# Performance work log

Hardware: AMD Instinct MI355X
Metric: run time of the kernel (lower is better)

Reference implementation:

```python
import jax, jax.numpy as jnp
import numpy as np
from jax import lax

K = 3
K2 = 9
PAD = 1
GN_GROUPS = 32
GN_EPS = 1e-5
COS_EPS = 1e-8


def conv2d(x, w):
    # 3x3, stride 1, pad 1, NCHW/OIHW
    return lax.conv_general_dilated(x, w, (1, 1), ((PAD, PAD), (PAD, PAD)),
                                    dimension_numbers=('NCHW', 'OIHW', 'NCHW'))


def group_norm(x, gamma, beta):
    N, C, H, W = x.shape
    xg = x.reshape(N, GN_GROUPS, C // GN_GROUPS, H, W)
    m = xg.mean(axis=(2, 3, 4), keepdims=True)
    v = xg.var(axis=(2, 3, 4), keepdims=True)
    xn = ((xg - m) * lax.rsqrt(v + GN_EPS)).reshape(N, C, H, W)
    return xn * gamma[None, :, None, None] + beta[None, :, None, None]


def deform_conv(x, offset, weight):
    # mmcv DeformConv, deformable_groups=1: offset [N, 2*K2, H, W] as (dy,dx) per kernel tap.
    N, C, H, W = x.shape
    off = offset.reshape(N, K2, 2, H, W)
    dy, dx = off[:, :, 0], off[:, :, 1]              # [N,K2,H,W]
    ky, kx = jnp.meshgrid(jnp.arange(K), jnp.arange(K), indexing='ij')
    ky = ky.reshape(K2).astype(x.dtype)
    kx = kx.reshape(K2).astype(x.dtype)
    hh = jnp.arange(H, dtype=x.dtype)
    ww = jnp.arange(W, dtype=x.dtype)
    # absolute (fractional) sample positions per output pixel and kernel tap
    py = hh[None, None, :, None] - PAD + ky[None, :, None, None] + dy   # [N,K2,H,W]
    px = ww[None, None, None, :] - PAD + kx[None, :, None, None] + dx
    y0 = jnp.floor(py)
    x0 = jnp.floor(px)
    ay = py - y0
    ax = px - x0
    xf = x.reshape(N, C, H * W)
    sampled = jnp.zeros((N, C, K2, H, W), x.dtype)
    for oy, wy in ((y0, 1.0 - ay), (y0 + 1.0, ay)):
        for ox, wx in ((x0, 1.0 - ax), (x0 + 1.0, ax)):
            valid = (oy >= 0) & (oy <= H - 1) & (ox >= 0) & (ox <= W - 1)
            yi = jnp.clip(oy, 0, H - 1).astype(jnp.int32)
            xi = jnp.clip(ox, 0, W - 1).astype(jnp.int32)
            idx = (yi * W + xi).reshape(N, 1, K2 * H * W)
            v = jnp.take_along_axis(xf, idx, axis=2).reshape(N, C, K2, H, W)
            w = jnp.where(valid, wy * wx, 0.0)[:, None]   # zero padding outside
            sampled = sampled + v * w
    O = weight.shape[0]
    return jnp.einsum('nckhw,ock->nohw', sampled, weight.reshape(O, C, K2))


def cos_sim(a, b):
    num = jnp.sum(a * b, axis=1)
    na = jnp.sqrt(jnp.sum(a * a, axis=1))
    nb = jnp.sqrt(jnp.sum(b * b, axis=1))
    return num / jnp.maximum(na * nb, COS_EPS)   # [N,H,W]


def agg(support, reference, layers):
    f = jnp.concatenate([support, reference], axis=1)
    for ow, ob, dw, gg, gb in layers[:3]:
        off = conv2d(f, ow) + ob[None, :, None, None]
        f = jax.nn.relu(group_norm(deform_conv(f, off, dw), gg, gb))
    ow, ob, dw, gg, gb = layers[3]
    off = conv2d(f, ow) + ob[None, :, None, None]
    return jax.nn.relu(group_norm(deform_conv(support, off, dw), gg, gb))


def setup_inputs() -> dict:
    key = jax.random.key(0)
    ks = jax.random.split(key, 16)
    C_in, C_out, H, W = 512, 256, 96, 96
    rn = lambda k, shape, s: jax.random.normal(k, shape, jnp.float32) * s
    inp = {'datas': jax.random.normal(ks[0], (2, C_out, H, W), jnp.float32)}
    i = 1
    for n in (1, 2, 3):
        inp[f'off{n}_w'] = rn(ks[i], (18, C_in, 3, 3), 0.01); i += 1
        inp[f'off{n}_b'] = jnp.zeros((18,), jnp.float32)
        inp[f'dcn{n}_w'] = rn(ks[i], (C_in, C_in, 3, 3), 0.02); i += 1
        inp[f'gn{n}_g'] = jnp.ones((C_in,), jnp.float32)
        inp[f'gn{n}_b'] = jnp.zeros((C_in,), jnp.float32)
    inp['off4_w'] = rn(ks[i], (18, C_in, 3, 3), 0.01); i += 1
    inp['off4_b'] = jnp.zeros((18,), jnp.float32)
    inp['dcn4_w'] = rn(ks[i], (C_out, C_out, 3, 3), 0.02); i += 1
    inp['gn4_g'] = jnp.ones((C_out,), jnp.float32)
    inp['gn4_b'] = jnp.zeros((C_out,), jnp.float32)
    return inp


def reference(datas, off1_w, off1_b, dcn1_w, gn1_g, gn1_b,
              off2_w, off2_b, dcn2_w, gn2_g, gn2_b,
              off3_w, off3_b, dcn3_w, gn3_g, gn3_b,
              off4_w, off4_b, dcn4_w, gn4_g, gn4_b):
    layers = [(off1_w, off1_b, dcn1_w, gn1_g, gn1_b),
              (off2_w, off2_b, dcn2_w, gn2_g, gn2_b),
              (off3_w, off3_b, dcn3_w, gn3_g, gn3_b),
              (off4_w, off4_b, dcn4_w, gn4_g, gn4_b)]
    support = datas[:1]
    reference_f = datas[1:]
    tt = agg(reference_f, reference_f, layers)   # [1,C_out,H,W]
    ttw = cos_sim(tt, tt)[:, None]               # [1,1,H,W]
    tk = agg(support, reference_f, layers)
    tkw = cos_sim(tt, tk)[:, None]
    w = jax.nn.softmax(jnp.stack([ttw, tkw], axis=0), axis=0)  # [2,1,1,H,W]
    f = jnp.stack([tt, tk], axis=0)                            # [2,1,C,H,W]
    return jnp.sum(w * f, axis=0)
```

## Files before the change

### kernel.cpp

```cpp
#include <hip/hip_runtime.h>
#include <math.h>

#define HW 9216
#define WIDTH 96
#define FSTRIDE (512*HW)
#define RSTRIDE (256*HW)
#define TABSTRIDE (9*HW)
#define PXP 12544
#define FTPROWS 12800

typedef __attribute__((ext_vector_type(8))) short bf16x8;
typedef __attribute__((ext_vector_type(4))) float f32x4;
typedef __attribute__((ext_vector_type(8))) unsigned short u16x8;

__device__ __forceinline__ unsigned short f2bf(float f) {
  unsigned int u = __float_as_uint(f);
  u += 0x7FFFu + ((u >> 16) & 1u);
  return (unsigned short)(u >> 16);
}
__device__ __forceinline__ float bf2f(unsigned short s) {
  return __uint_as_float(((unsigned int)s) << 16);
}

#define GLDS(g, l) __builtin_amdgcn_global_load_lds( \
    (const __attribute__((address_space(1))) unsigned int*)(g), \
    (__attribute__((address_space(3))) unsigned int*)(l), 16, 0, 0)

__global__ void k_zero(unsigned short* p, unsigned int n8) {
  unsigned int i = blockIdx.x * 256 + threadIdx.x;
  if (i < n8) ((u16x8*)p)[i] = (u16x8){0, 0, 0, 0, 0, 0, 0, 0};
}

__global__ void __launch_bounds__(256) k_mkftp_cat(
    const float* __restrict__ lo0, const float* __restrict__ lo1,
    const float* __restrict__ hi, unsigned short* __restrict__ dst,
    int C, int CB) {
  const int b = blockIdx.z;
  const float* lo = b ? lo1 : lo0;
  unsigned short* d = dst + (size_t)b * FTPROWS * C + 128 * C;
  const int px0 = blockIdx.x * 64, c0 = blockIdx.y * 64;
  __shared__ float tile[64][65];
  const int t = threadIdx.x;
#pragma unroll
  for (int rep = 0; rep < 16; ++rep) {
    int idx = rep * 256 + t;
    int cl = idx >> 6, pl = idx & 63;
    int cg = c0 + cl;
    const float* s = (cg < CB) ? (lo + (size_t)cg * HW) : (hi + (size_t)(cg - CB) * HW);
    tile[cl][pl] = s[px0 + pl];
  }
  __syncthreads();
  const int pl = t >> 2, cu = (t & 3) * 16;
  const int px = px0 + pl;
  const int h = px / WIDTH, w = px - h * WIDTH;
  const size_t pxp = (size_t)(h + 1) * 128 + (w + 1);
  u16x8 o0, o1;
#pragma unroll
  for (int j = 0; j < 8; ++j) o0[j] = f2bf(tile[cu + j][pl]);
#pragma unroll
  for (int j = 0; j < 8; ++j) o1[j] = f2bf(tile[cu + 8 + j][pl]);
  unsigned short* p = d + pxp * C + c0 + cu;
  *(u16x8*)p = o0;
  *(u16x8*)(p + 8) = o1;
}

__global__ void __launch_bounds__(256) k_mkftp_gn(
    const unsigned short* __restrict__ yh, const float2* __restrict__ stat,
    const float* __restrict__ gamma, const float* __restrict__ beta,
    unsigned short* __restrict__ dst) {
  const int C = 512;
  const int b = blockIdx.z;
  unsigned short* d = dst + (size_t)b * FTPROWS * C + 128 * C;
  const int px0 = blockIdx.x * 64, c0 = blockIdx.y * 64;
  __shared__ float tile[64][65];
  const int t = threadIdx.x;
#pragma unroll
  for (int rep = 0; rep < 16; ++rep) {
    int idx = rep * 256 + t;
    int cl = idx >> 6, pl = idx & 63;
    int cg = c0 + cl;
    float2 st = stat[b * 32 + (cg >> 4)];
    float v = bf2f(yh[(size_t)b * FSTRIDE + (size_t)cg * HW + px0 + pl]);
    v = (v - st.x) * st.y * gamma[cg] + beta[cg];
    tile[cl][pl] = fmaxf(v, 0.f);
  }
  __syncthreads();
  const int pl = t >> 2, cu = (t & 3) * 16;
  const int px = px0 + pl;
  const int h = px / WIDTH, w = px - h * WIDTH;
  const size_t pxp = (size_t)(h + 1) * 128 + (w + 1);
  u16x8 o0, o1;
#pragma unroll
  for (int j = 0; j < 8; ++j) o0[j] = f2bf(tile[cu + j][pl]);
#pragma unroll
  for (int j = 0; j < 8; ++j) o1[j] = f2bf(tile[cu + 8 + j][pl]);
  unsigned short* p = d + pxp * C + c0 + cu;
  *(u16x8*)p = o0;
  *(u16x8*)(p + 8) = o1;
}

__global__ void k_prepW(const float* __restrict__ ow, unsigned short* __restrict__ Wt) {
  int i = blockIdx.x * 256 + threadIdx.x;
  int k = i / (32 * 512), r = i - k * 32 * 512;
  int oc = r / 512, c = r - oc * 512;
  Wt[i] = (oc < 18) ? f2bf(ow[((size_t)oc * 512 + c) * 9 + k]) : (unsigned short)0;
}

__global__ void __launch_bounds__(256) k_offmm(const unsigned short* __restrict__ ftp,
                                               const unsigned short* __restrict__ Wt,
                                               float* __restrict__ part) {
  const int C = 512;
  __shared__ unsigned short As[2][128 * 64];
  __shared__ unsigned short Bs[2][32 * 64];
  const int tid = threadIdx.x;
  const int lane = tid & 63, wv = tid >> 6;
  const int b = blockIdx.z, ks = blockIdx.y;
  const int pxp0 = 128 + blockIdx.x * 128;
  const unsigned short* fb = ftp + (size_t)b * FTPROWS * C + 128 * C;

  const int lr = lane >> 3;
  const int lu = lane & 7;
  const int fr = lane & 15, hi = lane >> 4;

  f32x4 acc[2][2];
#pragma unroll
  for (int i = 0; i < 2; ++i)
#pragma unroll
    for (int j = 0; j < 2; ++j) acc[i][j] = (f32x4){0.f, 0.f, 0.f, 0.f};

#define OFFMM_STAGE(S, BUF)                                                   \
  {                                                                           \
    const int k_ = ks * 3 + ((S) >> 3);                                       \
    const int dlt_ = (k_ / 3 - 1) * 128 + (k_ % 3 - 1);                       \
    const int c0_ = ((S) & 7) * 64;                                           \
    _Pragma("unroll")                                                         \
    for (int q = 0; q < 4; ++q) {                                             \
      int row = wv * 32 + q * 8 + lr;                                         \
      int su = lu ^ (row & 7);                                                \
      GLDS(fb + (size_t)(pxp0 + dlt_ + row) * C + c0_ + su * 8,               \
           (char*)&As[BUF][0] + (wv * 32 + q * 8) * 128);                     \
    }                                                                         \
    {                                                                         \
      int row = wv * 8 + lr;                                                  \
      int su = lu ^ (row & 7);                                                \
      GLDS(Wt + ((size_t)k_ * 32 + row) * C + c0_ + su * 8,                   \
           (char*)&Bs[BUF][0] + wv * 8 * 128);                                \
    }                                                                         \
  }

  OFFMM_STAGE(0, 0);
  for (int s = 0; s < 24; ++s) {
    const int cur = s & 1;
    if (s + 1 < 24) {
      OFFMM_STAGE(s + 1, cur ^ 1);
      asm volatile("s_waitcnt vmcnt(5)" ::: "memory");
    } else {
      asm volatile("s_waitcnt vmcnt(0)" ::: "memory");
    }
    __builtin_amdgcn_s_barrier();
#pragma unroll
    for (int kk = 0; kk < 2; ++kk) {
      bf16x8 a[2], bb[2];
#pragma unroll
      for (int i = 0; i < 2; ++i) {
        int row = wv * 32 + i * 16 + fr;
        a[i] = *(const bf16x8*)&As[cur][row * 64 + (((kk * 4 + hi) ^ (row & 7)) * 8)];
      }
#pragma unroll
      for (int j = 0; j < 2; ++j) {
        int row = j * 16 + fr;
        bb[j] = *(const bf16x8*)&Bs[cur][row * 64 + (((kk * 4 + hi) ^ (row & 7)) * 8)];
      }
#pragma unroll
      for (int i = 0; i < 2; ++i)
#pragma unroll
        for (int j = 0; j < 2; ++j)
          acc[i][j] = __builtin_amdgcn_mfma_f32_16x16x32_bf16(a[i], bb[j], acc[i][j], 0, 0, 0);
    }
    __builtin_amdgcn_s_barrier();
  }

  float* pb = part + ((size_t)(b * 3 + ks)) * PXP * 32;
#pragma unroll
  for (int i = 0; i < 2; ++i)
#pragma unroll
    for (int j = 0; j < 2; ++j) {
      int row0 = pxp0 + wv * 32 + i * 16 + hi * 4;
      int col = j * 16 + fr;
#pragma unroll
      for (int q = 0; q < 4; ++q)
        pb[(size_t)(row0 + q) * 32 + col] = acc[i][j][q];
    }
}

__global__ void k_table(const float* __restrict__ part, const float* __restrict__ ob,
                        int4* __restrict__ tabi, float4* __restrict__ tabw) {
  int b = blockIdx.z, k = blockIdx.y;
  int px = blockIdx.x * 256 + threadIdx.x;
  int h = px / WIDTH, w = px - h * WIDTH;
  size_t pxp = (size_t)(h + 1) * 128 + (w + 1);
  const float* pb = part + (size_t)b * 3 * PXP * 32 + pxp * 32;
  float dy = ob[2 * k] + pb[2 * k] + pb[(size_t)PXP * 32 + 2 * k] + pb[2 * (size_t)PXP * 32 + 2 * k];
  float dx = ob[2 * k + 1] + pb[2 * k + 1] + pb[(size_t)PXP * 32 + 2 * k + 1] + pb[2 * (size_t)PXP * 32 + 2 * k + 1];
  float py = (float)(h - 1 + k / 3) + dy;
  float pxx = (float)(w - 1 + k % 3) + dx;
  float y0 = floorf(py), x0 = floorf(pxx);
  float ay = py - y0, ax = pxx - x0;
  float wy[2] = {1.f - ay, ay}, wx[2] = {1.f - ax, ax};
  int idx[4]; float wt[4];
#pragma unroll
  for (int t = 0; t < 4; ++t) {
    float oy = y0 + (float)(t >> 1);
    float ox = x0 + (float)(t & 1);
    bool valid = (oy >= 0.f) && (oy <= 95.f) && (ox >= 0.f) && (ox <= 95.f);
    int yi = (int)fminf(fmaxf(oy, 0.f), 95.f);
    int xi = (int)fminf(fmaxf(ox, 0.f), 95.f);
    idx[t] = (yi + 1) * 128 + (xi + 1);
    wt[t] = valid ? wy[t >> 1] * wx[t & 1] : 0.f;
  }
  size_t e = (size_t)b * TABSTRIDE + (size_t)k * HW + px;
  tabi[e] = make_int4(idx[0], idx[1], idx[2], idx[3]);
  tabw[e] = make_float4(wt[0], wt[1], wt[2], wt[3]);
}

__global__ void __launch_bounds__(256) k_sample_t(
    const unsigned short* __restrict__ ftp,
    const int4* __restrict__ tabi, const float4* __restrict__ tabw,
    unsigned short* __restrict__ samp, int C, int kbase, int rowK) {
  const int z = blockIdx.z;
  const int b = z & 1, kloc = z >> 1;
  const int k = kbase + kloc;
  const int t = threadIdx.x;
  const int px = blockIdx.x * 64 + (t >> 2);
  const int c = blockIdx.y * 64 + (t & 3) * 16;
  const unsigned short* fb = ftp + (size_t)b * FTPROWS * C + 128 * C;
  size_t e = (size_t)b * TABSTRIDE + (size_t)k * HW + px;
  int4 id = tabi[e];
  float4 wt = tabw[e];
  float acc[16];
#pragma unroll
  for (int j = 0; j < 16; ++j) acc[j] = 0.f;
  const int ids[4] = {id.x, id.y, id.z, id.w};
  const float wts[4] = {wt.x, wt.y, wt.z, wt.w};
#pragma unroll
  for (int s = 0; s < 4; ++s) {
    const unsigned short* p = fb + (size_t)ids[s] * C + c;
    u16x8 v0 = *(const u16x8*)p;
    u16x8 v1 = *(const u16x8*)(p + 8);
    float wgt = wts[s];
#pragma unroll
    for (int j = 0; j < 8; ++j) acc[j] += wgt * bf2f(v0[j]);
#pragma unroll
    for (int j = 0; j < 8; ++j) acc[8 + j] += wgt * bf2f(v1[j]);
  }
  u16x8 o0, o1;
#pragma unroll
  for (int j = 0; j < 8; ++j) o0[j] = f2bf(acc[j]);
#pragma unroll
  for (int j = 0; j < 8; ++j) o1[j] = f2bf(acc[8 + j]);
  unsigned short* dst = samp + ((size_t)b * HW + px) * rowK + kloc * C + c;
  *(u16x8*)dst = o0;
  *(u16x8*)(dst + 8) = o1;
}

__global__ void k_prepA(const float* __restrict__ dw, unsigned short* __restrict__ Ap,
                        int C) {
  int o = blockIdx.x * 256 + threadIdx.x;
  int K = 9 * C;
  int m = o / K, r = o - m * K;
  int k = r / C, c = r - k * C;
  Ap[o] = f2bf(dw[((size_t)m * C + c) * 9 + k]);
}

__device__ __forceinline__ void stage_ab96(const unsigned short* __restrict__ Ag,
                                           const unsigned short* __restrict__ Bg,
                                           int lda, int rowK, int kt,
                                           unsigned short* as_, unsigned short* bs_,
                                           int wv, int lane) {
  const int lr = lane >> 2;
  const int lu = lane & 3;
#pragma unroll
  for (int q = 0; q < 2; ++q) {
    int row = wv * 32 + q * 16 + lr;
    int su = lu ^ ((row >> 1) & 3);
    GLDS(Ag + (size_t)row * lda + kt + su * 8, (char*)as_ + (wv * 2 + q) * 1024);
  }
  const int nb = (wv < 2) ? 2 : 1;
  const int bu0 = (wv < 2) ? (2 * wv) : (wv + 2);
  for (int q = 0; q < nb; ++q) {
    int unit = bu0 + q;
    int row = unit * 16 + lr;
    int su = lu ^ ((row >> 1) & 3);
    GLDS(Bg + (size_t)row * rowK + kt + su * 8, (char*)bs_ + unit * 1024);
  }
}

__global__ void __launch_bounds__(256) k_dcgemm(
    const unsigned short* __restrict__ Ap, const unsigned short* __restrict__ Bt,
    unsigned short* __restrict__ Yh, float2* __restrict__ gnp,
    int lda, int rowK, int aOff, int accum, int CperG, int dogn) {
  __shared__ unsigned short As[3][128 * 32];
  __shared__ unsigned short Bs[3][96 * 32];
  const int tid = threadIdx.x;
  const int lane = tid & 63, wv = tid >> 6;

  const int nwg = gridDim.x;
  const int cpx = nwg >> 3;
  const int bid = blockIdx.x;
  const int l = (bid & 7) * cpx + (bid >> 3);
  const int nm = nwg / 192;
  const int m_i = l % nm;
  const int rest = l / nm;
  const int n_i = rest % 96;
  const int b = rest / 96;

  const int m0 = m_i << 7, n0 = n_i * 96;
  const unsigned short* Ag = Ap + (size_t)m0 * lda + aOff;
  const unsigned short* Bg = Bt + ((size_t)b * HW + n0) * rowK;

  const int wm = (wv >> 1) * 64, wn = (wv & 1) * 48;
  const int fr = lane & 15, hi = lane >> 4;
  const int nt = rowK >> 5;

  f32x4 acc[4][3];
#pragma unroll
  for (int i = 0; i < 4; ++i)
#pragma unroll
    for (int j = 0; j < 3; ++j) acc[i][j] = (f32x4){0.f, 0.f, 0.f, 0.f};

  stage_ab96(Ag, Bg, lda, rowK, 0,  &As[0][0], &Bs[0][0], wv, lane);
  stage_ab96(Ag, Bg, lda, rowK, 32, &As[1][0], &Bs[1][0], wv, lane);

  for (int t = 0; t < nt; ++t) {
    const int cur = t % 3;
    if (t + 2 < nt) {
      stage_ab96(Ag, Bg, lda, rowK, (t + 2) << 5, &As[(t + 2) % 3][0],
                 &Bs[(t + 2) % 3][0], wv, lane);
      if (wv < 2) asm volatile("s_waitcnt vmcnt(8)" ::: "memory");
      else        asm volatile("s_waitcnt vmcnt(6)" ::: "memory");
    } else if (t + 1 < nt) {
      if (wv < 2) asm volatile("s_waitcnt vmcnt(4)" ::: "memory");
      else        asm volatile("s_waitcnt vmcnt(3)" ::: "memory");
    } else {
      asm volatile("s_waitcnt vmcnt(0)" ::: "memory");
    }
    __builtin_amdgcn_s_barrier();
    __builtin_amdgcn_sched_barrier(0);
    bf16x8 a[4], bb[3];
#pragma unroll
    for (int i = 0; i < 4; ++i) {
      int row = wm + i * 16 + fr;
      a[i] = *(const bf16x8*)&As[cur][row * 32 + ((hi ^ ((row >> 1) & 3)) * 8)];
    }
#pragma unroll
    for (int j = 0; j < 3; ++j) {
      int row = wn + j * 16 + fr;
      bb[j] = *(const bf16x8*)&Bs[cur][row * 32 + ((hi ^ ((row >> 1) & 3)) * 8)];
    }
    __builtin_amdgcn_s_setprio(1);
#pragma unroll
    for (int i = 0; i < 4; ++i)
#pragma unroll
      for (int j = 0; j < 3; ++j)
        acc[i][j] = __builtin_amdgcn_mfma_f32_16x16x32_bf16(a[i], bb[j], acc[i][j], 0, 0, 0);
    __builtin_amdgcn_s_setprio(0);
    __builtin_amdgcn_s_barrier();
  }

  unsigned short* Yb = Yh + (size_t)b * FSTRIDE;
  const int orow = m0 + wm + hi * 4;
  const int ocol = n0 + wn + fr;
  float s_[4], q_[4];
#pragma unroll
  for (int i = 0; i < 4; ++i) { s_[i] = 0.f; q_[i] = 0.f; }
#pragma unroll
  for (int i = 0; i < 4; ++i) {
#pragma unroll
    for (int j = 0; j < 3; ++j) {
      unsigned short* p = Yb + (size_t)(orow + i * 16) * HW + ocol + j * 16;
#pragma unroll
      for (int q = 0; q < 4; ++q) {
        float v = acc[i][j][q];
        if (accum) v += bf2f(p[(size_t)q * HW]);
        p[(size_t)q * HW] = f2bf(v);
        s_[i] += v;
        q_[i] += v * v;
      }
    }
  }

  if (dogn) {
    const int redmax = (CperG == 16) ? 32 : 16;
#pragma unroll
    for (int i = 0; i < 4; ++i) {
      float s = s_[i], q = q_[i];
      for (int off = 1; off <= redmax; off <<= 1) {
        s += __shfl_xor(s, off);
        q += __shfl_xor(q, off);
      }
      int row0 = m0 + wm + i * 16 + ((CperG == 8) ? (lane >> 5) * 8 : 0);
      int g = row0 / CperG;
      bool writer = (CperG == 16) ? (lane == 0) : ((lane & 31) == 0);
      if (writer)
        gnp[(((size_t)(b * 32 + g)) * 96 + n_i) * 2 + (wv & 1)] = make_float2(s, q);
    }
  }
}

__global__ void k_gnfin2(const float2* __restrict__ gnp, float2* __restrict__ stat,
                         int CperG) {
  int t = threadIdx.x;
  float s = 0.f, q = 0.f;
  for (int j = 0; j < 192; ++j) {
    float2 v = gnp[(size_t)t * 192 + j];
    s += v.x; q += v.y;
  }
  float n = (float)(CperG * HW);
  float m = s / n;
  float var = q / n - m * m;
  stat[t] = make_float2(m, rsqrtf(var + 1e-5f));
}

__global__ void __launch_bounds__(256) k_gnstats1h(const unsigned short* __restrict__ yh,
                                                   float2* __restrict__ part, int CperG) {
  const int b = blockIdx.z, g = blockIdx.x, ch = blockIdx.y;
  const int n = CperG * HW;
  const int cs8 = (n >> 4) >> 3;
  const u16x8* p = (const u16x8*)(yh + (size_t)b * FSTRIDE + (size_t)g * n + (size_t)ch * (n >> 4));
  float s = 0.f, q = 0.f;
  for (int i = threadIdx.x; i < cs8; i += 256) {
    u16x8 v = p[i];
#pragma unroll
    for (int j = 0; j < 8; ++j) { float f = bf2f(v[j]); s += f; q += f * f; }
  }
  __shared__ float ss[256], qs[256];
  ss[threadIdx.x] = s; qs[threadIdx.x] = q;
  __syncthreads();
  for (int d = 128; d > 0; d >>= 1) {
    if (threadIdx.x < d) { ss[threadIdx.x] += ss[threadIdx.x + d]; qs[threadIdx.x] += qs[threadIdx.x + d]; }
    __syncthreads();
  }
  if (threadIdx.x == 0) part[((b << 5) + g) * 16 + ch] = make_float2(ss[0], qs[0]);
}

__global__ void k_gnfin(const float2* __restrict__ part, float2* __restrict__ stat,
                        int CperG) {
  int t = threadIdx.x;
  float s = 0.f, q = 0.f;
#pragma unroll
  for (int j = 0; j < 16; ++j) { float2 v = part[t * 16 + j]; s += v.x; q += v.y; }
  float n = (float)(CperG * HW);
  float m = s / n;
  float var = q / n - m * m;
  stat[t] = make_float2(m, rsqrtf(var + 1e-5f));
}

__global__ void __launch_bounds__(256) k_gncos(
    const unsigned short* __restrict__ yh, const float2* __restrict__ stat,
    const float* __restrict__ gamma, const float* __restrict__ beta,
    float* __restrict__ res, float4* __restrict__ cospart) {
  int px = blockIdx.x * 256 + threadIdx.x;
  int cc = blockIdx.y;
  float saa = 0.f, sbb = 0.f, sab = 0.f;
  for (int c = cc * 32; c < cc * 32 + 32; ++c) {
    float2 st0 = stat[c >> 3];
    float2 st1 = stat[32 + (c >> 3)];
    float ga = gamma[c], be = beta[c];
    float a = fmaxf((bf2f(yh[(size_t)c * HW + px]) - st0.x) * st0.y * ga + be, 0.f);
    float b = fmaxf((bf2f(yh[(size_t)FSTRIDE + (size_t)c * HW + px]) - st1.x) * st1.y * ga + be, 0.f);
    res[(size_t)c * HW + px] = a;
    res[(size_t)RSTRIDE + (size_t)c * HW + px] = b;
    saa += a * a; sbb += b * b; sab += a * b;
  }
  cospart[(size_t)cc * HW + px] = make_float4(saa, sbb, sab, 0.f);
}

__global__ void k_cos2(const float4* __restrict__ part, float* __restrict__ wpix) {
  int px = blockIdx.x * 256 + threadIdx.x;
  float saa = 0.f, sbb = 0.f, sab = 0.f;
#pragma unroll
  for (int cc = 0; cc < 8; ++cc) {
    float4 v = part[(size_t)cc * HW + px];
    saa += v.x; sbb += v.y; sab += v.z;
  }
  float na = sqrtf(saa), nb = sqrtf(sbb);
  float ttw = saa / fmaxf(na * na, 1e-8f);
  float tkw = sab / fmaxf(na * nb, 1e-8f);
  float m = fmaxf(ttw, tkw);
  float e0 = expf(ttw - m), e1 = expf(tkw - m);
  wpix[px] = e0 / (e0 + e1);
}

__global__ void k_combine(const float* __restrict__ res, const float* __restrict__ wpix,
                          float* __restrict__ out) {
  int i = blockIdx.x * 256 + threadIdx.x;
  int px = i % HW;
  float w0 = wpix[px];
  out[i] = w0 * res[i] + (1.f - w0) * res[(size_t)RSTRIDE + i];
}

extern "C" void kernel_launch(void* const* d_in, const int* in_sizes, int n_in,
                              void* d_out, int out_size, void* d_ws, size_t ws_size,
                              hipStream_t stream) {
  const float* datas = (const float*)d_in[0];
  const float* ow[4] = {(const float*)d_in[1], (const float*)d_in[6],
                        (const float*)d_in[11], (const float*)d_in[16]};
  const float* ob[4] = {(const float*)d_in[2], (const float*)d_in[7],
                        (const float*)d_in[12], (const float*)d_in[17]};
  const float* dw[4] = {(const float*)d_in[3], (const float*)d_in[8],
                        (const float*)d_in[13], (const float*)d_in[18]};
  const float* gg[4] = {(const float*)d_in[4], (const float*)d_in[9],
                        (const float*)d_in[14], (const float*)d_in[19]};
  const float* gb[4] = {(const float*)d_in[5], (const float*)d_in[10],
                        (const float*)d_in[15], (const float*)d_in[20]};

  const int fullk = (ws_size >= 236400000ull) ? 1 : 0;
  const size_t sampN = fullk ? (2 * (size_t)HW * 4608) : (2 * (size_t)HW * 1536);

  float* ws = (float*)d_ws;
  unsigned short* yh = (unsigned short*)ws;
  float* offp3 = ws + (2 * (size_t)FSTRIDE * 2) / 4;
  float4* tabw = (float4*)(offp3 + 2 * 3 * (size_t)PXP * 32);
  int4*   tabi = (int4*)(tabw + 2 * (size_t)TABSTRIDE);
  float* wpix = (float*)(tabi + 2 * (size_t)TABSTRIDE);
  float2* stat = (float2*)(wpix + HW);
  float2* gnp  = stat + 64;
  float2* gnpart = gnp + 2 * 32 * 96 * 2;
  float4* cospart = (float4*)(gnpart + 1024);
  float* endp = (float*)(cospart + 8 * (size_t)HW);
  size_t ofs = ((size_t)(endp - ws) + 3) & ~(size_t)3;
  unsigned short* samp = (unsigned short*)(ws + ofs);
  unsigned short* Ap = samp + sampN;
  unsigned short* Wt = Ap + (size_t)512 * 4608;
  unsigned short* ftp512 = Wt + (size_t)9 * 32 * 512;
  unsigned short* ftp256 = fullk ? (samp + 2 * (size_t)HW * 2304)
                                 : (ftp512 + 2 * (size_t)FTPROWS * 512);
  float* res = (float*)(ftp256 + 2 * (size_t)FTPROWS * 256);

  dim3 blk(256);
  k_zero<<<dim3(2 * FTPROWS * 512 / 8 / 256), blk, 0, stream>>>(ftp512, 2u * FTPROWS * 512 / 8);

  for (int lyr = 0; lyr < 4; ++lyr) {
    const int Cx = (lyr < 3) ? 512 : 256;
    const int M  = Cx;
    const int CperG = (lyr < 3) ? 16 : 8;
    if (lyr == 0) {
      k_mkftp_cat<<<dim3(144, 8, 2), blk, 0, stream>>>(datas + RSTRIDE, datas,
                                                       datas + RSTRIDE, ftp512, 512, 256);
    } else {
      k_mkftp_gn<<<dim3(144, 8, 2), blk, 0, stream>>>(yh, stat, gg[lyr - 1], gb[lyr - 1],
                                                      ftp512);
    }
    k_prepA<<<dim3(M * 9 * Cx / 256), blk, 0, stream>>>(dw[lyr], Ap, Cx);
    k_prepW<<<dim3(9 * 32 * 512 / 256), blk, 0, stream>>>(ow[lyr], Wt);
    k_offmm<<<dim3(96, 3, 2), blk, 0, stream>>>(ftp512, Wt, offp3);
    k_table<<<dim3(36, 9, 2), blk, 0, stream>>>(offp3, ob[lyr], tabi, tabw);
    const unsigned short* sftp;
    if (lyr < 3) {
      sftp = ftp512;
    } else {
      k_zero<<<dim3(2 * FTPROWS * 256 / 8 / 256), blk, 0, stream>>>(ftp256, 2u * FTPROWS * 256 / 8);
      k_mkftp_cat<<<dim3(144, 4, 2), blk, 0, stream>>>(datas + RSTRIDE, datas,
                                                       datas, ftp256, 256, 256);
      sftp = ftp256;
    }
    const int nch = fullk ? 1 : 3;
    const int nk = 9 / nch;
    const int rowK = nk * Cx;
    for (int ch = 0; ch < nch; ++ch) {
      k_sample_t<<<dim3(144, Cx / 64, 2 * nk), blk, 0, stream>>>(sftp, tabi, tabw, samp,
                                                                 Cx, ch * nk, rowK);
      k_dcgemm<<<dim3((M / 128) * 96 * 2), blk, 0, stream>>>(
          Ap, samp, yh, gnp, 9 * Cx, rowK, ch * rowK, ch > 0, CperG,
          fullk && (ch == nch - 1));
    }
    if (fullk) {
      k_gnfin2<<<dim3(1), dim3(64), 0, stream>>>(gnp, stat, CperG);
    } else {
      k_gnstats1h<<<dim3(32, 16, 2), blk, 0, stream>>>(yh, gnpart, CperG);
      k_gnfin<<<dim3(1), dim3(64), 0, stream>>>(gnpart, stat, CperG);
    }
  }

  k_gncos<<<dim3(36, 8), blk, 0, stream>>>(yh, stat, gg[3], gb[3], res, cospart);
  k_cos2<<<dim3(36), blk, 0, stream>>>(cospart, wpix);
  k_combine<<<dim3(RSTRIDE / 256), blk, 0, stream>>>(res, wpix, (float*)d_out);
}
```

Before: 979.5 us.

## Batch weight prep for all layers and widen sampling kernel with XCD-aware block mapping

Converts all four layers' deform and offset conv weights to bf16 in one launch each at the start, replacing per-layer prep launches. The bilinear sampling kernel now has each thread handle 32 channels instead of 16, reusing each table lookup across more channels. Blocks are flattened into a 1D grid and remapped so that consecutive logical tiles land on the same XCD, aiming for better L2 locality. The fullk workspace threshold is raised to make room for the larger all-layer weight buffers, which could push some configurations onto the chunked path.

After: 1.060 ms. 1.08x slower.

```diff
diff --git a/kernel.cpp b/kernel.cpp
--- a/kernel.cpp
+++ b/kernel.cpp
@@ -99,11 +99,29 @@
   *(u16x8*)(p + 8) = o1;
 }
 
-__global__ void k_prepW(const float* __restrict__ ow, unsigned short* __restrict__ Wt) {
+__global__ void k_prepW_all(const float* __restrict__ ow0, const float* __restrict__ ow1,
+                            const float* __restrict__ ow2, const float* __restrict__ ow3,
+                            unsigned short* __restrict__ wt) {
   int i = blockIdx.x * 256 + threadIdx.x;
-  int k = i / (32 * 512), r = i - k * 32 * 512;
+  int lyr = i / 147456, r0 = i % 147456;
+  const float* ow = (lyr == 0) ? ow0 : (lyr == 1) ? ow1 : (lyr == 2) ? ow2 : ow3;
+  int k = r0 / (32 * 512), r = r0 - k * 32 * 512;
   int oc = r / 512, c = r - oc * 512;
-  Wt[i] = (oc < 18) ? f2bf(ow[((size_t)oc * 512 + c) * 9 + k]) : (unsigned short)0;
+  wt[i] = (oc < 18) ? f2bf(ow[((size_t)oc * 512 + c) * 9 + k]) : (unsigned short)0;
+}
+
+__global__ void k_prepA_all(const float* __restrict__ dw0, const float* __restrict__ dw1,
+                            const float* __restrict__ dw2, const float* __restrict__ dw3,
+                            unsigned short* __restrict__ ap) {
+  int i = blockIdx.x * 256 + threadIdx.x;
+  int lyr, o, C; size_t base;
+  if (i < 7077888) { lyr = i / 2359296; o = i % 2359296; C = 512; base = (size_t)lyr * 2359296; }
+  else             { lyr = 3; o = i - 7077888; C = 256; base = 7077888; }
+  const float* dw = (lyr == 0) ? dw0 : (lyr == 1) ? dw1 : (lyr == 2) ? dw2 : dw3;
+  int K = 9 * C;
+  int m = o / K, r = o - m * K;
+  int k = r / C, c = r - k * C;
+  ap[base + o] = f2bf(dw[((size_t)m * C + c) * 9 + k]);
 }
 
 __global__ void __launch_bounds__(256) k_offmm(const unsigned short* __restrict__ ftp,
@@ -223,53 +241,51 @@
   tabw[e] = make_float4(wt[0], wt[1], wt[2], wt[3]);
 }
 
-__global__ void __launch_bounds__(256) k_sample_t(
+__global__ void __launch_bounds__(256) k_sample2(
     const unsigned short* __restrict__ ftp,
     const int4* __restrict__ tabi, const float4* __restrict__ tabw,
-    unsigned short* __restrict__ samp, int C, int kbase, int rowK) {
-  const int z = blockIdx.z;
-  const int b = z & 1, kloc = z >> 1;
+    unsigned short* __restrict__ samp, int C, int kbase, int rowK, int yc) {
+  const int nwg = gridDim.x;
+  const int cpx = nwg >> 3;
+  const int bid = blockIdx.x;
+  const int l = (bid & 7) * cpx + (bid >> 3);
+  const int ci = l % yc;
+  const int r = l / yc;
+  const int pxi = r % 144;
+  const int zk = r / 144;
+  const int b = zk & 1, kloc = zk >> 1;
   const int k = kbase + kloc;
   const int t = threadIdx.x;
-  const int px = blockIdx.x * 64 + (t >> 2);
-  const int c = blockIdx.y * 64 + (t & 3) * 16;
+  const int px = pxi * 64 + (t >> 2);
+  const int c = ci * 128 + (t & 3) * 32;
   const unsigned short* fb = ftp + (size_t)b * FTPROWS * C + 128 * C;
   size_t e = (size_t)b * TABSTRIDE + (size_t)k * HW + px;
   int4 id = tabi[e];
   float4 wt = tabw[e];
-  float acc[16];
-#pragma unroll
-  for (int j = 0; j < 16; ++j) acc[j] = 0.f;
+  float acc[32];
+#pragma unroll
+  for (int j = 0; j < 32; ++j) acc[j] = 0.f;
   const int ids[4] = {id.x, id.y, id.z, id.w};
   const float wts[4] = {wt.x, wt.y, wt.z, wt.w};
 #pragma unroll
   for (int s = 0; s < 4; ++s) {
     const unsigned short* p = fb + (size_t)ids[s] * C + c;
-    u16x8 v0 = *(const u16x8*)p;
-    u16x8 v1 = *(const u16x8*)(p + 8);
     float wgt = wts[s];
 #pragma unroll
-    for (int j = 0; j < 8; ++j) acc[j] += wgt * bf2f(v0[j]);
-#pragma unroll
-    for (int j = 0; j < 8; ++j) acc[8 + j] += wgt * bf2f(v1[j]);
-  }
-  u16x8 o0, o1;
-#pragma unroll
-  for (int j = 0; j < 8; ++j) o0[j] = f2bf(acc[j]);
-#pragma unroll
-  for (int j = 0; j < 8; ++j) o1[j] = f2bf(acc[8 + j]);
+    for (int v = 0; v < 4; ++v) {
+      u16x8 vv = *(const u16x8*)(p + v * 8);
+#pragma unroll
+      for (int j = 0; j < 8; ++j) acc[v * 8 + j] += wgt * bf2f(vv[j]);
+    }
+  }
   unsigned short* dst = samp + ((size_t)b * HW + px) * rowK + kloc * C + c;
-  *(u16x8*)dst = o0;
-  *(u16x8*)(dst + 8) = o1;
-}
-
-__global__ void k_prepA(const float* __restrict__ dw, unsigned short* __restrict__ Ap,
-                        int C) {
-  int o = blockIdx.x * 256 + threadIdx.x;
-  int K = 9 * C;
-  int m = o / K, r = o - m * K;
-  int k = r / C, c = r - k * C;
-  Ap[o] = f2bf(dw[((size_t)m * C + c) * 9 + k]);
+#pragma unroll
+  for (int v = 0; v < 4; ++v) {
+    u16x8 o;
+#pragma unroll
+    for (int j = 0; j < 8; ++j) o[j] = f2bf(acc[v * 8 + j]);
+    *(u16x8*)(dst + v * 8) = o;
+  }
 }
 
 __device__ __forceinline__ void stage_ab96(const unsigned short* __restrict__ Ag,
@@ -514,7 +530,7 @@
   const float* gb[4] = {(const float*)d_in[5], (const float*)d_in[10],
                         (const float*)d_in[15], (const float*)d_in[20]};
 
-  const int fullk = (ws_size >= 236400000ull) ? 1 : 0;
+  const int fullk = (ws_size >= 248500000ull) ? 1 : 0;
   const size_t sampN = fullk ? (2 * (size_t)HW * 4608) : (2 * (size_t)HW * 1536);
 
   float* ws = (float*)d_ws;
@@ -530,20 +546,25 @@
   float* endp = (float*)(cospart + 8 * (size_t)HW);
   size_t ofs = ((size_t)(endp - ws) + 3) & ~(size_t)3;
   unsigned short* samp = (unsigned short*)(ws + ofs);
-  unsigned short* Ap = samp + sampN;
-  unsigned short* Wt = Ap + (size_t)512 * 4608;
-  unsigned short* ftp512 = Wt + (size_t)9 * 32 * 512;
+  unsigned short* apAll = samp + sampN;
+  unsigned short* wtAll = apAll + (size_t)7667712;
+  unsigned short* ftp512 = wtAll + (size_t)589824;
   unsigned short* ftp256 = fullk ? (samp + 2 * (size_t)HW * 2304)
                                  : (ftp512 + 2 * (size_t)FTPROWS * 512);
   float* res = (float*)(ftp256 + 2 * (size_t)FTPROWS * 256);
 
   dim3 blk(256);
   k_zero<<<dim3(2 * FTPROWS * 512 / 8 / 256), blk, 0, stream>>>(ftp512, 2u * FTPROWS * 512 / 8);
+  k_prepA_all<<<dim3(29952), blk, 0, stream>>>(dw[0], dw[1], dw[2], dw[3], apAll);
+  k_prepW_all<<<dim3(2304), blk, 0, stream>>>(ow[0], ow[1], ow[2], ow[3], wtAll);
 
   for (int lyr = 0; lyr < 4; ++lyr) {
     const int Cx = (lyr < 3) ? 512 : 256;
     const int M  = Cx;
     const int CperG = (lyr < 3) ? 16 : 8;
+    const unsigned short* Ap = (lyr < 3) ? (apAll + (size_t)lyr * 2359296)
+                                         : (apAll + (size_t)7077888);
+    const unsigned short* Wt = wtAll + (size_t)lyr * 147456;
     if (lyr == 0) {
       k_mkftp_cat<<<dim3(144, 8, 2), blk, 0, stream>>>(datas + RSTRIDE, datas,
                                                        datas + RSTRIDE, ftp512, 512, 256);
@@ -551,8 +572,6 @@
       k_mkftp_gn<<<dim3(144, 8, 2), blk, 0, stream>>>(yh, stat, gg[lyr - 1], gb[lyr - 1],
                                                       ftp512);
     }
-    k_prepA<<<dim3(M * 9 * Cx / 256), blk, 0, stream>>>(dw[lyr], Ap, Cx);
-    k_prepW<<<dim3(9 * 32 * 512 / 256), blk, 0, stream>>>(ow[lyr], Wt);
     k_offmm<<<dim3(96, 3, 2), blk, 0, stream>>>(ftp512, Wt, offp3);
     k_table<<<dim3(36, 9, 2), blk, 0, stream>>>(offp3, ob[lyr], tabi, tabw);
     const unsigned short* sftp;
@@ -567,9 +586,10 @@
     const int nch = fullk ? 1 : 3;
     const int nk = 9 / nch;
     const int rowK = nk * Cx;
+    const int yc = Cx / 128;
     for (int ch = 0; ch < nch; ++ch) {
-      k_sample_t<<<dim3(144, Cx / 64, 2 * nk), blk, 0, stream>>>(sftp, tabi, tabw, samp,
-                                                                 Cx, ch * nk, rowK);
+      k_sample2<<<dim3(144 * yc * 2 * nk), blk, 0, stream>>>(sftp, tabi, tabw, samp,
+                                                             Cx, ch * nk, rowK, yc);
       k_dcgemm<<<dim3((M / 128) * 96 * 2), blk, 0, stream>>>(
           Ap, samp, yh, gnp, 9 * Cx, rowK, ch * rowK, ch > 0, CperG,
           fullk && (ch == nch - 1));
```
